# Performance work log

Measured on AMD Instinct MI355X. Metric: run time of the kernel, lower is better.

The kernel has to match this reference:

```python
import jax, jax.numpy as jnp
import numpy as np

XI = 4.0  # init kwarg


def _gaussian_kernel(xi: float):
    radius = int(3 * xi)
    coords = jnp.arange(-radius, radius + 1, dtype=jnp.float32)
    g1 = jnp.exp(-coords ** 2 / (2 * xi * xi))
    g1 = g1 / g1.sum()
    # dense 3D outer-product kernel, shape (K, K, K)
    g3 = g1[:, None, None] * g1[None, :, None] * g1[None, None, :]
    K = g3.shape[0]
    # grouped depthwise weight: (out=3, in/groups=1, K, K, K)
    return jnp.broadcast_to(g3[None, None], (3, 1, K, K, K))


def setup_inputs() -> dict:
    key = jax.random.key(0)
    x = jax.random.normal(key, (1, 3, 160, 160, 160), dtype=jnp.float32)
    kernel = _gaussian_kernel(XI)
    return {"x": x, "kernel": kernel}


def reference(x, kernel):
    # grouped Conv3d, groups=3 (depthwise), 'same' padding of radius each side
    r = (kernel.shape[-1] - 1) // 2
    return jax.lax.conv_general_dilated(
        x, kernel,
        window_strides=(1, 1, 1),
        padding=[(r, r), (r, r), (r, r)],
        dimension_numbers=("NCDHW", "OIDHW", "NCDHW"),
        feature_group_count=3,
    )
```

## Files before the change

### kernel.cpp

```cpp
#include <hip/hip_runtime.h>
#include <hip/hip_fp16.h>


#define NV 160
constexpr int KS    = 25;
constexpr int RAD   = 12;
constexpr int PLANE = NV * NV;
constexpr int VOL   = NV * NV * NV;
constexpr int TOT   = 3 * VOL;
constexpr int ROWS  = NV + 2 * RAD;

constexpr int PITCH = 17;
constexpr int OPT   = 10;
constexpr int WIN   = OPT + KS - 1;
constexpr int OROW  = 168;

constexpr int HC2    = 80;
constexpr int TR     = 104;
constexpr int TPW    = 80;
constexpr int VROWS  = 92;
constexpr int VSLOTS = VROWS * 20;
constexpr int ZSLOTS = 12 * 20;

__device__ __forceinline__ void pk(float2& a, float2 g, float2 v) {
    asm("v_pk_fma_f32 %0, %1, %2, %0" : "+v"(a) : "v"(g), "v"(v));
}

__device__ __forceinline__ void load_g(const float* __restrict__ k3, float* g) {
    float c   = k3[12 * 625 + 312];
    float g12 = cbrtf(c);
    float inv = 1.0f / (g12 * g12);
#pragma unroll
    for (int t = 0; t < KS; ++t) g[t] = k3[t * 625 + 312] * inv;
}

__device__ __forceinline__ void gll16(const void* g, void* l) {
    __builtin_amdgcn_global_load_lds(
        (const __attribute__((address_space(1))) void*)g,
        (__attribute__((address_space(3))) void*)l, 16, 0, 0);
}

__global__ __launch_bounds__(256) void conv_w(const float* __restrict__ in,
                                              __half* __restrict__ out,
                                              const float* __restrict__ k3) {
    __shared__ float2 T[ROWS][PITCH];
    float gs[KS];
    load_g(k3, gs);
    float2 g2[KS];
#pragma unroll
    for (int t = 0; t < KS; ++t) g2[t] = make_float2(gs[t], gs[t]);

    int tid = threadIdx.x;
    int b   = blockIdx.x;
    int ht  = b % 5;
    int cd  = b / 5;
    int h0  = ht * 32;
    const float* base = in + (size_t)cd * PLANE;

    int wl = tid & 31, hq = tid >> 5;
#pragma unroll
    for (int hh = 0; hh < 2; ++hh) {
        int hp = hq + hh * 8;
        const float* r0 = base + (h0 + 2 * hp) * NV;
#pragma unroll
        for (int ib = 0; ib < ROWS; ib += 32) {
            int i = ib + wl;
            if (i < ROWS) {
                int wv = i - RAD;
                float a = 0.f, bb = 0.f;
                if (wv >= 0 && wv < NV) { a = r0[wv]; bb = r0[NV + wv]; }
                T[i][hp] = make_float2(a, bb);
            }
        }
    }
    __syncthreads();

    int p  = tid & 15;
    int ct = tid >> 4;
    int wb = ct * OPT;
    float2 acc[OPT];
#pragma unroll
    for (int j = 0; j < OPT; ++j) acc[j] = make_float2(0.f, 0.f);
#pragma unroll
    for (int it = 0; it < WIN; ++it) {
        float2 v = T[wb + it][p];
#pragma unroll
        for (int j = 0; j < OPT; ++j) {
            int t = it - j;
            if (t >= 0 && t < KS) pk(acc[j], g2[t], v);
        }
    }

    __syncthreads();
    __half* Ost = (__half*)(&T[0][0]);
#pragma unroll
    for (int j = 0; j < OPT; ++j) {
        Ost[(2 * p)     * OROW + wb + j] = __float2half_rn(acc[j].x);
        Ost[(2 * p + 1) * OROW + wb + j] = __float2half_rn(acc[j].y);
    }
    __syncthreads();
    __half* ob = out + (size_t)cd * PLANE + (size_t)h0 * NV;
#pragma unroll
    for (int it = 0; it < 3; ++it) {
        int task = it * 256 + tid;
        if (task < 640) {
            int chunk = task % 20, row = task / 20;
            uint4 v = *(const uint4*)(Ost + row * OROW + 8 * chunk);
            *(uint4*)(ob + (size_t)row * NV + 8 * chunk) = v;
        }
    }
}

__global__ __launch_bounds__(320) void conv_h(const __half* __restrict__ in,
                                              __half* __restrict__ out,
                                              const float* __restrict__ k3) {
    __shared__ __half2 T[TR][TPW];
    float gs[KS];
    load_g(k3, gs);
    float2 g2[KS];
#pragma unroll
    for (int t = 0; t < KS; ++t) g2[t] = make_float2(gs[t], gs[t]);

    int tid = threadIdx.x;
    int b   = blockIdx.x;
    int hh  = b & 1;
    int cd  = b >> 1;
    int h0  = hh * HC2;
    char* Tf = (char*)(&T[0][0]);

    int zbase = (hh == 0) ? 0 : 92 * 320;
    if (tid < ZSLOTS)
        *(uint4*)(Tf + zbase + tid * 16) = make_uint4(0u, 0u, 0u, 0u);

    int vbase = (hh == 0) ? 12 * 320 : 0;
    const char* gsrc = (const char*)(in + (size_t)cd * PLANE
                                     + (size_t)((hh == 0) ? 0 : 68) * NV);
    int wavebase = tid & ~63;
#pragma unroll
    for (int it = 0; it < 4; ++it) {
        int sw = it * 320 + wavebase;
        gll16(gsrc + (size_t)(sw + (tid & 63)) * 16, Tf + vbase + sw * 16);
    }
#pragma unroll
    for (int it = 4; it < 6; ++it) {
        int slot = it * 320 + tid;
        if (slot < VSLOTS) {
            int sw = it * 320 + wavebase;
            gll16(gsrc + (size_t)slot * 16, Tf + vbase + sw * 16);
        }
    }
    asm volatile("s_waitcnt vmcnt(2) lgkmcnt(0)" ::: "memory");
    __builtin_amdgcn_s_barrier();
    __builtin_amdgcn_sched_barrier(0);

    int wp = tid % 80, oc = tid / 80;
    {
        int rb = oc * OPT;
        float2 acc[OPT];
#pragma unroll
        for (int j = 0; j < OPT; ++j) acc[j] = make_float2(0.f, 0.f);
#pragma unroll
        for (int it = 0; it < WIN; ++it) {
            float2 v = __half22float2(T[rb + it][wp]);
#pragma unroll
            for (int j = 0; j < OPT; ++j) {
                int t = it - j;
                if (t >= 0 && t < KS) pk(acc[j], g2[t], v);
            }
        }
        __half* op = out + (size_t)cd * PLANE + (size_t)(h0 + rb) * NV + 2 * wp;
#pragma unroll
        for (int j = 0; j < OPT; ++j)
            *(__half2*)(op + j * NV) = __float22half2_rn(acc[j]);
    }
    __builtin_amdgcn_sched_barrier(0);
    asm volatile("s_waitcnt vmcnt(0)" ::: "memory");
    __builtin_amdgcn_s_barrier();
    __builtin_amdgcn_sched_barrier(0);
    {
        int rb = (oc + 4) * OPT;
        float2 acc[OPT];
#pragma unroll
        for (int j = 0; j < OPT; ++j) acc[j] = make_float2(0.f, 0.f);
#pragma unroll
        for (int it = 0; it < WIN; ++it) {
            float2 v = __half22float2(T[rb + it][wp]);
#pragma unroll
            for (int j = 0; j < OPT; ++j) {
                int t = it - j;
                if (t >= 0 && t < KS) pk(acc[j], g2[t], v);
            }
        }
        __half* op = out + (size_t)cd * PLANE + (size_t)(h0 + rb) * NV + 2 * wp;
#pragma unroll
        for (int j = 0; j < OPT; ++j)
            *(__half2*)(op + j * NV) = __float22half2_rn(acc[j]);
    }
}

__global__ __launch_bounds__(320) void conv_d(const __half* __restrict__ in,
                                              float* __restrict__ out,
                                              const float* __restrict__ k3) {
    __shared__ __half2 T[TR][TPW];
    float gs[KS];
    load_g(k3, gs);
    float2 g2[KS];
#pragma unroll
    for (int t = 0; t < KS; ++t) g2[t] = make_float2(gs[t], gs[t]);

    int tid = threadIdx.x;
    int b   = blockIdx.x;
    int dh  = b & 1;
    int ch  = b >> 1;
    int c   = ch / NV, h = ch % NV;
    int d0  = dh * HC2;
    char* Tf = (char*)(&T[0][0]);

    int zbase = (dh == 0) ? 0 : 92 * 320;
    if (tid < ZSLOTS)
        *(uint4*)(Tf + zbase + tid * 16) = make_uint4(0u, 0u, 0u, 0u);

    int vbase = (dh == 0) ? 12 * 320 : 0;
    int dg0   = (dh == 0) ? 0 : 68;
    const char* gd = (const char*)(in + (size_t)c * VOL + h * NV
                                   + (size_t)dg0 * PLANE);
    int wavebase = tid & ~63;
#pragma unroll
    for (int it = 0; it < 4; ++it) {
        int slot = it * 320 + tid;
        int rr = slot / 20, cc = slot % 20;
        int sw = it * 320 + wavebase;
        gll16(gd + (size_t)rr * (PLANE * 2) + cc * 16, Tf + vbase + sw * 16);
    }
#pragma unroll
    for (int it = 4; it < 6; ++it) {
        int slot = it * 320 + tid;
        if (slot < VSLOTS) {
            int rr = slot / 20, cc = slot % 20;
            int sw = it * 320 + wavebase;
            gll16(gd + (size_t)rr * (PLANE * 2) + cc * 16, Tf + vbase + sw * 16);
        }
    }
    asm volatile("s_waitcnt vmcnt(2) lgkmcnt(0)" ::: "memory");
    __builtin_amdgcn_s_barrier();
    __builtin_amdgcn_sched_barrier(0);

    int wp = tid % 80, oc = tid / 80;
    {
        int rb = oc * OPT;
        float2 acc[OPT];
#pragma unroll
        for (int j = 0; j < OPT; ++j) acc[j] = make_float2(0.f, 0.f);
#pragma unroll
        for (int it = 0; it < WIN; ++it) {
            float2 v = __half22float2(T[rb + it][wp]);
#pragma unroll
            for (int j = 0; j < OPT; ++j) {
                int t = it - j;
                if (t >= 0 && t < KS) pk(acc[j], g2[t], v);
            }
        }
        float* op = out + (size_t)c * VOL + h * NV + 2 * wp;
#pragma unroll
        for (int j = 0; j < OPT; ++j)
            *(float2*)(op + (size_t)(d0 + rb + j) * PLANE) = acc[j];
    }
    __builtin_amdgcn_sched_barrier(0);
    asm volatile("s_waitcnt vmcnt(0)" ::: "memory");
    __builtin_amdgcn_s_barrier();
    __builtin_amdgcn_sched_barrier(0);
    {
        int rb = (oc + 4) * OPT;
        float2 acc[OPT];
#pragma unroll
        for (int j = 0; j < OPT; ++j) acc[j] = make_float2(0.f, 0.f);
#pragma unroll
        for (int it = 0; it < WIN; ++it) {
            float2 v = __half22float2(T[rb + it][wp]);
#pragma unroll
            for (int j = 0; j < OPT; ++j) {
                int t = it - j;
                if (t >= 0 && t < KS) pk(acc[j], g2[t], v);
            }
        }
        float* op = out + (size_t)c * VOL + h * NV + 2 * wp;
#pragma unroll
        for (int j = 0; j < OPT; ++j)
            *(float2*)(op + (size_t)(d0 + rb + j) * PLANE) = acc[j];
    }
}

__global__ __launch_bounds__(256) void conv3d_direct(const float* __restrict__ x,
                                                     const float* __restrict__ k3,
                                                     float* __restrict__ out) {
    int idx = blockIdx.x * 256 + threadIdx.x;
    if (idx >= TOT) return;
    int w = idx % NV;
    int t = idx / NV;
    int h = t % NV; t /= NV;
    int d = t % NV;
    int c = t / NV;
    const float* kc = k3 + c * (KS * KS * KS);
    float acc = 0.f;
    for (int i = 0; i < KS; ++i) {
        int dd = d + i - RAD;
        if (dd < 0 || dd >= NV) continue;
        for (int j = 0; j < KS; ++j) {
            int hh = h + j - RAD;
            if (hh < 0 || hh >= NV) continue;
            const float* xr = x + (c * NV + dd) * NV * NV + hh * NV + (w - RAD);
            const float* kr = kc + (i * KS + j) * KS;
            int k0 = (RAD - w) > 0 ? (RAD - w) : 0;
            int k1 = (NV + RAD - w) < KS ? (NV + RAD - w) : KS;
            for (int k = k0; k < k1; ++k) acc += kr[k] * xr[k];
        }
    }
    out[idx] = acc;
}

extern "C" void kernel_launch(void* const* d_in, const int* in_sizes, int n_in,
                              void* d_out, int out_size, void* d_ws, size_t ws_size,
                              hipStream_t stream) {
    const float* x  = (const float*)d_in[0];
    const float* k3 = (const float*)d_in[1];
    float* out = (float*)d_out;

    if (ws_size >= (size_t)TOT * 2 * sizeof(__half)) {
        __half* tmpA = (__half*)d_ws;
        __half* tmpB = tmpA + TOT;
        conv_w<<<2400, 256, 0, stream>>>(x, tmpA, k3);
        conv_h<<<480 * 2, 320, 0, stream>>>(tmpA, tmpB, k3);
        conv_d<<<480 * 2, 320, 0, stream>>>(tmpB, out, k3);
    } else {
        conv3d_direct<<<(TOT + 255) / 256, 256, 0, stream>>>(x, k3, out);
    }
}
```

Baseline: 52.83 us.

## Rework W-pass conv to async LDS load, row-major tile and direct half2 stores

The first (W-axis) pass now stages a 32x160 row-major fp32 tile into LDS with global_load_lds 16-byte async copies instead of a transposed padded float2 tile filled by scalar loads. Each thread convolves 10 consecutive outputs along a row with scalar FMAs, using a symmetric 13-tap weight table and clamped, masked reads for the halo. It writes fp16 pairs directly to global memory, dropping the LDS transpose and restage step. This loses the packed FMA and adds per-tap clamp and select work, and same-row LDS reads with a stride of 10 floats may cause bank conflicts.

After: 51.87 us, median of 2. No clear change (-1.8%).

```diff
diff --git a/kernel.cpp b/kernel.cpp
--- a/kernel.cpp
+++ b/kernel.cpp
@@ -8,12 +8,10 @@
 constexpr int PLANE = NV * NV;
 constexpr int VOL   = NV * NV * NV;
 constexpr int TOT   = 3 * VOL;
-constexpr int ROWS  = NV + 2 * RAD;
-
-constexpr int PITCH = 17;
+
+constexpr int WR    = 32;
 constexpr int OPT   = 10;
 constexpr int WIN   = OPT + KS - 1;
-constexpr int OROW  = 168;
 
 constexpr int HC2    = 80;
 constexpr int TR     = 104;
@@ -22,6 +20,8 @@
 constexpr int VSLOTS = VROWS * 20;
 constexpr int ZSLOTS = 12 * 20;
 
+#define GWS(t) gs[(t) < 13 ? (t) : 24 - (t)]
+
 __device__ __forceinline__ void pk(float2& a, float2 g, float2 v) {
     asm("v_pk_fma_f32 %0, %1, %2, %0" : "+v"(a) : "v"(g), "v"(v));
 }
@@ -34,6 +34,14 @@
     for (int t = 0; t < KS; ++t) g[t] = k3[t * 625 + 312] * inv;
 }
 
+__device__ __forceinline__ void load_g13(const float* __restrict__ k3, float* g) {
+    float c   = k3[12 * 625 + 312];
+    float g12 = cbrtf(c);
+    float inv = 1.0f / (g12 * g12);
+#pragma unroll
+    for (int t = 0; t < 13; ++t) g[t] = k3[t * 625 + 312] * inv;
+}
+
 __device__ __forceinline__ void gll16(const void* g, void* l) {
     __builtin_amdgcn_global_load_lds(
         (const __attribute__((address_space(1))) void*)g,
@@ -43,71 +51,52 @@
 __global__ __launch_bounds__(256) void conv_w(const float* __restrict__ in,
                                               __half* __restrict__ out,
                                               const float* __restrict__ k3) {
-    __shared__ float2 T[ROWS][PITCH];
-    float gs[KS];
-    load_g(k3, gs);
-    float2 g2[KS];
-#pragma unroll
-    for (int t = 0; t < KS; ++t) g2[t] = make_float2(gs[t], gs[t]);
+    __shared__ float X[WR][NV];
+    float gs[13];
+    load_g13(k3, gs);
 
     int tid = threadIdx.x;
     int b   = blockIdx.x;
-    int ht  = b % 5;
+    int hc  = b % 5;
     int cd  = b / 5;
-    int h0  = ht * 32;
-    const float* base = in + (size_t)cd * PLANE;
-
-    int wl = tid & 31, hq = tid >> 5;
-#pragma unroll
-    for (int hh = 0; hh < 2; ++hh) {
-        int hp = hq + hh * 8;
-        const float* r0 = base + (h0 + 2 * hp) * NV;
-#pragma unroll
-        for (int ib = 0; ib < ROWS; ib += 32) {
-            int i = ib + wl;
-            if (i < ROWS) {
-                int wv = i - RAD;
-                float a = 0.f, bb = 0.f;
-                if (wv >= 0 && wv < NV) { a = r0[wv]; bb = r0[NV + wv]; }
-                T[i][hp] = make_float2(a, bb);
-            }
-        }
+    int h0  = hc * WR;
+    const char* gsrc = (const char*)(in + (size_t)cd * PLANE + (size_t)h0 * NV);
+    char* Xf = (char*)(&X[0][0]);
+    int wavebase = tid & ~63;
+
+#pragma unroll
+    for (int it = 0; it < 5; ++it) {
+        int sw = it * 256 + wavebase;
+        gll16(gsrc + (size_t)(sw + (tid & 63)) * 16, Xf + sw * 16);
     }
     __syncthreads();
 
-    int p  = tid & 15;
-    int ct = tid >> 4;
-    int wb = ct * OPT;
-    float2 acc[OPT];
-#pragma unroll
-    for (int j = 0; j < OPT; ++j) acc[j] = make_float2(0.f, 0.f);
-#pragma unroll
-    for (int it = 0; it < WIN; ++it) {
-        float2 v = T[wb + it][p];
-#pragma unroll
-        for (int j = 0; j < OPT; ++j) {
-            int t = it - j;
-            if (t >= 0 && t < KS) pk(acc[j], g2[t], v);
-        }
-    }
-
-    __syncthreads();
-    __half* Ost = (__half*)(&T[0][0]);
-#pragma unroll
-    for (int j = 0; j < OPT; ++j) {
-        Ost[(2 * p)     * OROW + wb + j] = __float2half_rn(acc[j].x);
-        Ost[(2 * p + 1) * OROW + wb + j] = __float2half_rn(acc[j].y);
-    }
-    __syncthreads();
-    __half* ob = out + (size_t)cd * PLANE + (size_t)h0 * NV;
-#pragma unroll
-    for (int it = 0; it < 3; ++it) {
-        int task = it * 256 + tid;
-        if (task < 640) {
-            int chunk = task % 20, row = task / 20;
-            uint4 v = *(const uint4*)(Ost + row * OROW + 8 * chunk);
-            *(uint4*)(ob + (size_t)row * NV + 8 * chunk) = v;
-        }
+    int c  = tid & 15;
+    int rr = tid >> 4;
+
+#pragma unroll
+    for (int ph = 0; ph < 2; ++ph) {
+        int row = rr + 16 * ph;
+        float acc[OPT];
+#pragma unroll
+        for (int j = 0; j < OPT; ++j) acc[j] = 0.f;
+#pragma unroll
+        for (int it = 0; it < WIN; ++it) {
+            int wq = c * OPT + it - RAD;
+            int wc = min(max(wq, 0), NV - 1);
+            float v = X[row][wc];
+            v = (wq == wc) ? v : 0.f;
+#pragma unroll
+            for (int j = 0; j < OPT; ++j) {
+                int t = it - j;
+                if (t >= 0 && t < KS) acc[j] = fmaf(GWS(t), v, acc[j]);
+            }
+        }
+        __half* ob = out + (size_t)cd * PLANE + (size_t)(h0 + row) * NV + c * OPT;
+#pragma unroll
+        for (int j = 0; j < OPT / 2; ++j)
+            *(__half2*)(ob + 2 * j) =
+                __float22half2_rn(make_float2(acc[2 * j], acc[2 * j + 1]));
     }
 }
 
@@ -115,11 +104,11 @@
                                               __half* __restrict__ out,
                                               const float* __restrict__ k3) {
     __shared__ __half2 T[TR][TPW];
-    float gs[KS];
-    load_g(k3, gs);
+    float gsv[KS];
+    load_g(k3, gsv);
     float2 g2[KS];
 #pragma unroll
-    for (int t = 0; t < KS; ++t) g2[t] = make_float2(gs[t], gs[t]);
+    for (int t = 0; t < KS; ++t) g2[t] = make_float2(gsv[t], gsv[t]);
 
     int tid = threadIdx.x;
     int b   = blockIdx.x;
@@ -202,11 +191,11 @@
                                               float* __restrict__ out,
                                               const float* __restrict__ k3) {
     __shared__ __half2 T[TR][TPW];
-    float gs[KS];
-    load_g(k3, gs);
+    float gsv[KS];
+    load_g(k3, gsv);
     float2 g2[KS];
 #pragma unroll
-    for (int t = 0; t < KS; ++t) g2[t] = make_float2(gs[t], gs[t]);
+    for (int t = 0; t < KS; ++t) g2[t] = make_float2(gsv[t], gsv[t]);
 
     int tid = threadIdx.x;
     int b   = blockIdx.x;
@@ -328,7 +317,7 @@
     if (ws_size >= (size_t)TOT * 2 * sizeof(__half)) {
         __half* tmpA = (__half*)d_ws;
         __half* tmpB = tmpA + TOT;
-        conv_w<<<2400, 256, 0, stream>>>(x, tmpA, k3);
+        conv_w<<<480 * 5, 256, 0, stream>>>(x, tmpA, k3);
         conv_h<<<480 * 2, 320, 0, stream>>>(tmpA, tmpB, k3);
         conv_d<<<480 * 2, 320, 0, stream>>>(tmpB, out, k3);
     } else {
```
